# Kernel optimization log

Measured on AMD Instinct MI355X. Metric: run time of the kernel, lower is better.

## Reference

```python
import jax, jax.numpy as jnp
import numpy as np

B, IN, ED, PW, OUT, CL, NK = 2048, 4096, 8192, 2048, 256, 16, 32
MIX = 0.5

def _onehot_mask(key, n):
    # near-one-hot selector matrix [n, NK], as built by forward_update_masks
    idx = jax.random.choice(key, n, (NK,), replace=False)
    return jnp.zeros((n, NK), jnp.float32).at[idx, jnp.arange(NK)].set(1.0)

def setup_inputs():
    ks = jax.random.split(jax.random.key(0), 24)
    f = jnp.float32
    adj = (jax.random.uniform(ks[4], (IN, IN)) < 0.01).astype(f)
    adj = jnp.maximum(adj, adj.T).at[jnp.arange(IN), jnp.arange(IN)].set(1.0)
    return {
        'x_gene': jax.random.normal(ks[0], (B, IN), f),
        'x_invmea': jax.random.normal(ks[1], (B, IN), f),
        'x_curv': jax.random.normal(ks[2], (B, ED), f),
        'clinn': jax.random.normal(ks[3], (B, CL), f),
        'Adj': adj,
        'edge_mask': (jax.random.uniform(ks[5], (ED, IN)) < 0.005).astype(f),
        'pathway_mask': (jax.random.uniform(ks[6], (PW, ED)) < 0.02).astype(f),
        'top_gene_mask': _onehot_mask(ks[7], IN),
        'top_invmea_mask': _onehot_mask(ks[8], IN),
        'top_curv_mask': _onehot_mask(ks[9], ED),
        'top_path_mask': _onehot_mask(ks[10], PW),
        'W1': jnp.full((IN, IN), 0.05, f),
        'b1': 0.01 * jax.random.normal(ks[11], (IN,), f),
        'W2': jnp.full((ED, IN), 0.05, f),
        'b2': 0.01 * jax.random.normal(ks[12], (ED,), f),
        'W3': jnp.full((PW, ED), 0.05, f),
        'b3': 0.01 * jax.random.normal(ks[13], (PW,), f),
        'W4': 0.02 * jax.random.normal(ks[14], (OUT, PW), f),
        'b4': 0.01 * jax.random.normal(ks[15], (OUT,), f),
        'W5': 0.02 * jax.random.normal(ks[16], (OUT, OUT), f),
        'b5': 0.01 * jax.random.normal(ks[17], (OUT,), f),
        'W6': 0.05 * jax.random.normal(ks[18], (OUT, OUT + CL + 4 * NK), f),
        'W7': 0.05 * jax.random.normal(ks[19], (1, OUT), f),
        'mp11': MIX * jnp.ones(IN, f),
        'mp12': (1.0 - MIX) * jnp.ones(IN, f),
        'mp1': jnp.ones(IN, f),
        'mp21': MIX * jnp.ones(ED, f),
        'mp22': (1.0 - MIX) * jnp.ones(ED, f),
        'mp2': jnp.ones(ED, f),
        'mp3': jnp.ones(PW, f),
    }

def reference(x_gene, x_invmea, x_curv, clinn, Adj, edge_mask, pathway_mask,
              top_gene_mask, top_invmea_mask, top_curv_mask, top_path_mask,
              W1, b1, W2, b2, W3, b3, W4, b4, W5, b5, W6, W7,
              mp11, mp12, mp1, mp21, mp22, mp2, mp3):
    sg = jax.lax.stop_gradient
    sig = jax.nn.sigmoid
    kept_gene = sg(x_gene @ top_gene_mask)                     # [B,NK] gather-as-matmul
    x1 = sig(x_gene @ (W1 * Adj).T + b1)                       # masked linear [B,IN]
    x1 = x_invmea * (mp11 * mp1) + x1 * (mp12 * mp1)
    kept_invmea = sg(x1 @ top_invmea_mask)
    x1 = sig(x1 @ (W2 * edge_mask).T + b2)                     # [B,ED]
    x1 = x_curv * (mp21 * mp2) + x1 * (mp22 * mp2)
    kept_curv = sg(x1 @ top_curv_mask)
    x1 = sig(x1 @ (W3 * pathway_mask).T + b3)                  # [B,PW]
    x1 = x1 * mp3
    kept_path = sg(x1 @ top_path_mask)
    x1 = sig(x1 @ W4.T + b4)
    x1 = sig(x1 @ W5.T + b5)                                   # [B,OUT]
    x_cat = jnp.concatenate([x1, kept_gene, kept_invmea, kept_curv, kept_path, clinn], axis=1)
    lp = sig(x_cat @ W6.T)
    lp = lp - jnp.mean(lp, axis=1, keepdims=True)
    return lp @ W7.T                                           # [B,1]
```

## Files before the change

### kernel.cpp

```cpp
#include <hip/hip_runtime.h>

typedef unsigned short u16;
typedef __attribute__((ext_vector_type(4))) float f32x4;
typedef __attribute__((ext_vector_type(8))) short s16x8;

__device__ __forceinline__ u16 f2bf(float f) {
    union { float f; unsigned u; } c; c.f = f;
    return (u16)((c.u + 0x7fffu + ((c.u >> 16) & 1u)) >> 16);
}
__device__ __forceinline__ float bf2f(u16 u) {
    union { unsigned u; float f; } c; c.u = ((unsigned)u) << 16; return c.f;
}
__device__ __forceinline__ unsigned pk2(float a, float b) {
    return (unsigned)f2bf(a) | ((unsigned)f2bf(b) << 16);
}
__device__ __forceinline__ float sigm(float x) { return 1.0f / (1.0f + __expf(-x)); }
__device__ __forceinline__ void fma2(unsigned xv, float w, float& a0, float& a1) {
    union { float f; unsigned u; } lo, hi;
    lo.u = xv << 16; hi.u = xv & 0xFFFF0000u;
    a0 += w * lo.f; a1 += w * hi.f;
}

__device__ __forceinline__ void load16_g2l(const void* g, void* l) {
    __builtin_amdgcn_global_load_lds(
        (const __attribute__((address_space(1))) unsigned int*)(unsigned long long)g,
        (__attribute__((address_space(3))) unsigned int*)(unsigned int)(unsigned long long)l,
        16, 0, 0);
}

__device__ void d_transpF(const float* __restrict__ in, u16* __restrict__ out,
                          int Rr, int Cc, int bx, int by, float (*t)[65]) {
    const int r0 = by * 64, c0 = bx * 64;
    const int tid = threadIdx.x;
#pragma unroll
    for (int i = 0; i < 16; i++) {
        int idx = tid + i * 256;
        int rr = idx >> 6, cc = idx & 63;
        t[rr][cc] = in[(size_t)(r0 + rr) * Cc + c0 + cc];
    }
    __syncthreads();
#pragma unroll
    for (int i = 0; i < 16; i++) {
        int idx = tid + i * 256;
        int cc = idx >> 6, rr = idx & 63;
        out[(size_t)(c0 + cc) * Rr + r0 + rr] = f2bf(t[rr][cc]);
    }
}

__device__ void d_find(const float* __restrict__ mask, int n, int* __restrict__ outp,
                       int* red, int k) {
    int best = -1;
    for (int i = threadIdx.x; i < n; i += 256)
        if (mask[(size_t)i * 32 + k] != 0.0f) best = i;
    red[threadIdx.x] = best;
    __syncthreads();
    for (int off = 128; off > 0; off >>= 1) {
        if (threadIdx.x < off) {
            int o = red[threadIdx.x + off];
            if (o > red[threadIdx.x]) red[threadIdx.x] = o;
        }
        __syncthreads();
    }
    if (threadIdx.x == 0) *outp = red[0] < 0 ? 0 : red[0];
}

__device__ void d_conv(const float* __restrict__ in, u16* __restrict__ out,
                       int bid, unsigned n8) {
    unsigned i = bid * 256u + threadIdx.x;
    if (i >= n8) return;
    float4 a = ((const float4*)in)[2 * i];
    float4 b = ((const float4*)in)[2 * i + 1];
    uint4 o;
    o.x = pk2(a.x, a.y); o.y = pk2(a.z, a.w);
    o.z = pk2(b.x, b.y); o.w = pk2(b.z, b.w);
    ((uint4*)out)[i] = o;
}

template <int SUBC>
__device__ void d_ell_row(const float* __restrict__ M, const float* __restrict__ W,
                          unsigned* __restrict__ ell, int* __restrict__ cnt,
                          int PAD, int row, int* __restrict__ lds) {
    const int lane = threadIdx.x & 63;
    const int wv = threadIdx.x >> 6;
    const int C = SUBC * 4096;
    const float4* mrow = (const float4*)(M + (size_t)row * C);
    const float4* wrow = (const float4*)(W + (size_t)row * C);
    unsigned* erow = ell + (size_t)row * PAD;

    float4 m[SUBC * 4];
#pragma unroll
    for (int k = 0; k < SUBC * 4; k++) {
        int sc = k >> 2, i = k & 3;
        m[k] = mrow[(wv * SUBC + sc) * 256 + lane + i * 64];
    }
    unsigned bits[SUBC];
    int total = 0;
#pragma unroll
    for (int sc = 0; sc < SUBC; sc++) {
        unsigned b = 0;
#pragma unroll
        for (int i = 0; i < 4; i++) {
            const float4 mm = m[sc * 4 + i];
            if (mm.x != 0.f) b |= 1u << (4 * i);
            if (mm.y != 0.f) b |= 2u << (4 * i);
            if (mm.z != 0.f) b |= 4u << (4 * i);
            if (mm.w != 0.f) b |= 8u << (4 * i);
        }
        bits[sc] = b;
        total += __popc(b);
    }
    float4 w[SUBC * 4];
#pragma unroll
    for (int k = 0; k < SUBC * 4; k++) {
        int sc = k >> 2, i = k & 3;
        if ((bits[sc] >> (4 * i)) & 0xFu)
            w[k] = wrow[(wv * SUBC + sc) * 256 + lane + i * 64];
    }
    int pre = total;
#pragma unroll
    for (int off = 1; off < 64; off <<= 1) {
        int t = __shfl_up(pre, off, 64);
        if (lane >= off) pre += t;
    }
    if (lane == 63) lds[wv] = pre;
    __syncthreads();
    int base = 0;
#pragma unroll
    for (int v = 0; v < 3; v++) if (v < wv) base += lds[v];
    int s = base + pre - total;
    __asm__ volatile("" ::: "memory");
#pragma unroll
    for (int sc = 0; sc < SUBC; sc++) {
        const unsigned b = bits[sc];
        const int f4b = (wv * SUBC + sc) * 256;
#pragma unroll
        for (int i = 0; i < 4; i++) {
            if ((b >> (4 * i)) & 0xFu) {
                const float4 wv4 = w[sc * 4 + i];
                int c = (f4b + lane + i * 64) * 4;
                if (b & (1u << (4 * i))) { if (s < PAD) erow[s] = ((unsigned)f2bf(wv4.x) << 16) | (unsigned)(c + 0); s++; }
                if (b & (2u << (4 * i))) { if (s < PAD) erow[s] = ((unsigned)f2bf(wv4.y) << 16) | (unsigned)(c + 1); s++; }
                if (b & (4u << (4 * i))) { if (s < PAD) erow[s] = ((unsigned)f2bf(wv4.z) << 16) | (unsigned)(c + 2); s++; }
                if (b & (8u << (4 * i))) { if (s < PAD) erow[s] = ((unsigned)f2bf(wv4.w) << 16) | (unsigned)(c + 3); s++; }
            }
        }
    }
    if (threadIdx.x == 0) {
        int rt = lds[0] + lds[1] + lds[2] + lds[3];
        cnt[row] = rt > PAD ? PAD : rt;
    }
}

__global__ __launch_bounds__(256) void prep_all(
    const float* __restrict__ Adj, const float* __restrict__ W1,
    unsigned* __restrict__ ell1, int* __restrict__ cnt1,
    const float* __restrict__ edge, const float* __restrict__ W2,
    unsigned* __restrict__ ell2, int* __restrict__ cnt2,
    const float* __restrict__ path, const float* __restrict__ W3,
    unsigned* __restrict__ ell3, int* __restrict__ cnt3,
    const float* __restrict__ xg_f, const float* __restrict__ xinv_f,
    const float* __restrict__ xcv_f,
    u16* __restrict__ xTg, u16* __restrict__ xinvT, u16* __restrict__ xcvT,
    const float* __restrict__ m0, const float* __restrict__ m1,
    const float* __restrict__ m2, const float* __restrict__ m3,
    int* __restrict__ idx,
    const float* __restrict__ W4, u16* __restrict__ w4b,
    const float* __restrict__ W5, u16* __restrict__ w5b) {
    __shared__ float tile[64][65];
    const long long T = 22944, E = 14336;
    const int b = blockIdx.x;
    const int ea = (int)(((long long)b * E) / T);
    const int eb = (int)(((long long)(b + 1) * E) / T);
    if (eb > ea) {
        int id = ea;
        if (id < 4096) { d_ell_row<1>(Adj, W1, ell1, cnt1, 256, id, (int*)tile); return; }
        id -= 4096;
        if (id < 8192) { d_ell_row<1>(edge, W2, ell2, cnt2, 96, id, (int*)tile); return; }
        d_ell_row<2>(path, W3, ell3, cnt3, 320, id - 8192, (int*)tile);
        return;
    }
    int id = b - ea;
    if (id < 2048) { d_transpF(xg_f, xTg, 2048, 4096, id & 63, id >> 6, tile); return; }
    id -= 2048;
    if (id < 2048) { d_transpF(xinv_f, xinvT, 2048, 4096, id & 63, id >> 6, tile); return; }
    id -= 2048;
    if (id < 4096) { d_transpF(xcv_f, xcvT, 2048, 8192, id & 127, id >> 7, tile); return; }
    id -= 4096;
    if (id < 128) {
        const float* mk; int n;
        int which = id >> 5;
        if (which == 0)      { mk = m0; n = 4096; }
        else if (which == 1) { mk = m1; n = 4096; }
        else if (which == 2) { mk = m2; n = 8192; }
        else                 { mk = m3; n = 2048; }
        d_find(mk, n, idx + which * 32 + (id & 31), (int*)tile, id & 31);
        return;
    }
    id -= 128;
    if (id < 256) { d_conv(W4, w4b, id, 65536u); return; }
    id -= 256;
    d_conv(W5, w5b, id, 8192u);
}

template <int BPL>
__global__ __launch_bounds__(256) void spmm(const unsigned* __restrict__ ell,
                                            const int* __restrict__ cnt,
                                            const u16* __restrict__ xT,
                                            u16* __restrict__ outT,
                                            const float* __restrict__ bias,
                                            const float* __restrict__ c1a,
                                            const float* __restrict__ c1b,
                                            const float* __restrict__ c2a,
                                            const float* __restrict__ c2b,
                                            const u16* __restrict__ invT,
                                            const int* __restrict__ gidx,
                                            u16* __restrict__ gdst,
                                            int PAD) {
    const int lane = threadIdx.x & 63;
    const int wv = __builtin_amdgcn_readfirstlane((int)(threadIdx.x >> 6));
    const int j = blockIdx.y * 4 + wv;
    const int b0 = blockIdx.x * (64 * BPL) + lane * BPL;

    const unsigned* ep = ell + (size_t)j * PAD;
    int len = cnt[j];
    if (len > PAD) len = PAD;

    float acc[BPL];
#pragma unroll
    for (int i = 0; i < BPL; i++) acc[i] = 0.f;

    const int nfull = len >> 3;
    unsigned eA[8];
    if (nfull > 0) {
#pragma unroll
        for (int t = 0; t < 8; t++) eA[t] = ep[t];
    }
    for (int g = 0; g < nfull; g++) {
        unsigned eB[8];
        const bool more = (g + 1 < nfull);
        if (more) {
#pragma unroll
            for (int t = 0; t < 8; t++) eB[t] = ep[(g + 1) * 8 + t];
        }
        if (BPL == 8) {
            uint4 xv[8];
#pragma unroll
            for (int t = 0; t < 8; t++)
                xv[t] = *(const uint4*)(xT + ((size_t)(eA[t] & 0xFFFFu) << 11) + b0);
#pragma unroll
            for (int t = 0; t < 8; t++) {
                union { float f; unsigned u; } w; w.u = (eA[t] >> 16) << 16;
                fma2(xv[t].x, w.f, acc[0], acc[1]);
                fma2(xv[t].y, w.f, acc[2], acc[3]);
                fma2(xv[t].z, w.f, acc[4], acc[5]);
                fma2(xv[t].w, w.f, acc[6], acc[7]);
            }
        } else {
            uint2 xv[8];
#pragma unroll
            for (int t = 0; t < 8; t++)
                xv[t] = *(const uint2*)(xT + ((size_t)(eA[t] & 0xFFFFu) << 11) + b0);
#pragma unroll
            for (int t = 0; t < 8; t++) {
                union { float f; unsigned u; } w; w.u = (eA[t] >> 16) << 16;
                fma2(xv[t].x, w.f, acc[0], acc[1]);
                fma2(xv[t].y, w.f, acc[2], acc[3]);
            }
        }
        if (more) {
#pragma unroll
            for (int t = 0; t < 8; t++) eA[t] = eB[t];
        }
    }
    for (int s = nfull * 8; s < len; ++s) {
        unsigned e = ep[s];
        union { float f; unsigned u; } w; w.u = (e >> 16) << 16;
        const u16* xp = xT + ((size_t)(e & 0xFFFFu) << 11) + b0;
        if (BPL == 8) {
            uint4 xv = *(const uint4*)xp;
            fma2(xv.x, w.f, acc[0], acc[1]); fma2(xv.y, w.f, acc[2], acc[3]);
            fma2(xv.z, w.f, acc[4], acc[5]); fma2(xv.w, w.f, acc[6], acc[7]);
        } else {
            uint2 xv = *(const uint2*)xp;
            fma2(xv.x, w.f, acc[0], acc[1]); fma2(xv.y, w.f, acc[2], acc[3]);
        }
    }

    const float bi = bias[j];
    float c1 = 0.f;
    if (c1a) { c1 = c1a[j]; if (c1b) c1 *= c1b[j]; }
    float c2 = 1.f;
    if (c2a) { c2 = c2a[j]; if (c2b) c2 *= c2b[j]; }

    float v[BPL];
#pragma unroll
    for (int i = 0; i < BPL; i++) v[i] = sigm(acc[i] + bi) * c2;
    if (invT) {
        const unsigned long long* ip = (const unsigned long long*)(invT + ((size_t)j << 11) + b0);
#pragma unroll
        for (int h = 0; h < BPL / 4; h++) {
            unsigned long long iv = __builtin_nontemporal_load(ip + h);
            unsigned lo = (unsigned)iv, hi = (unsigned)(iv >> 32);
            union { float f; unsigned u; } g0, g1, g2, g3;
            g0.u = lo << 16; g1.u = lo & 0xFFFF0000u;
            g2.u = hi << 16; g3.u = hi & 0xFFFF0000u;
            v[4 * h + 0] += g0.f * c1; v[4 * h + 1] += g1.f * c1;
            v[4 * h + 2] += g2.f * c1; v[4 * h + 3] += g3.f * c1;
        }
    }
    unsigned long long pkv[BPL / 4];
#pragma unroll
    for (int h = 0; h < BPL / 4; h++)
        pkv[h] = (unsigned long long)pk2(v[4 * h + 0], v[4 * h + 1])
               | ((unsigned long long)pk2(v[4 * h + 2], v[4 * h + 3]) << 32);
    unsigned long long* op = (unsigned long long*)(outT + ((size_t)j << 11) + b0);
#pragma unroll
    for (int h = 0; h < BPL / 4; h++) __builtin_nontemporal_store(pkv[h], op + h);

    if (gdst) {
        for (int t = 0; t < 32; t++) {
            if (gidx[t] == j) {
                unsigned long long* gp = (unsigned long long*)(gdst + t * 2048 + b0);
#pragma unroll
                for (int h = 0; h < BPL / 4; h++) gp[h] = pkv[h];
            }
        }
    }
}

__global__ __launch_bounds__(256) void gatherFT(const float* __restrict__ src, int ld,
                                                const int* __restrict__ idx,
                                                u16* __restrict__ dstT) {
    int i = blockIdx.x * 256 + threadIdx.x;
    int kk = i >> 11, b = i & 2047;
    dstT[i] = f2bf(src[(size_t)b * ld + idx[kk]]);
}

__global__ __launch_bounds__(256) void transpB(const u16* __restrict__ in,
                                               u16* __restrict__ out, int Rr, int Cc) {
    __shared__ u16 t[64][66];
    const int r0 = blockIdx.y * 64, c0 = blockIdx.x * 64;
    const int tid = threadIdx.x;
#pragma unroll
    for (int i = 0; i < 16; i++) {
        int idx = tid + i * 256;
        int rr = idx >> 6, cc = idx & 63;
        t[rr][cc] = in[(size_t)(r0 + rr) * Cc + c0 + cc];
    }
    __syncthreads();
#pragma unroll
    for (int i = 0; i < 16; i++) {
        int idx = tid + i * 256;
        int cc = idx >> 6, rr = idx & 63;
        out[(size_t)(c0 + cc) * Rr + r0 + rr] = t[rr][cc];
    }
}

template <int WR, int WC, int MF, int NF, int KC, int WPE>
__global__ __launch_bounds__(WR * WC * 64, WPE)
void gemm_t(const u16* __restrict__ A, const u16* __restrict__ W,
            u16* __restrict__ Out, const float* __restrict__ bias, int N, int K) {
    constexpr int NTHR = WR * WC * 64;
    constexpr int BM = WR * MF * 16;
    constexpr int BN = WC * NF * 16;
    constexpr int BK = KC * 32;
    constexpr int CPR = KC * 4;
    constexpr int MSK = CPR - 1;
    constexpr int CA = BM * CPR / NTHR;
    constexpr int CB = BN * CPR / NTHR;
    constexpr int L  = CA + CB;

    __shared__ u16 At[2][BM * BK];
    __shared__ u16 Bt[2][BN * BK];

    const int tid = threadIdx.x;
    const int lane = tid & 63;
    const int wave = tid >> 6;
    const int wr = wave / WC, wc = wave % WC;
    const int tn = blockIdx.x, tm = blockIdx.y;
    const int r16 = lane & 15;
    const int q = lane >> 4;

    const u16* aSrc[CA]; int aDst[CA];
#pragma unroll
    for (int j = 0; j < CA; j++) {
        int c = tid + j * NTHR;
        int r = c / CPR, p = c - r * CPR;
        aSrc[j] = A + (size_t)(tm * BM + r) * K + (p ^ (r & MSK)) * 8;
        aDst[j] = c * 8;
    }
    const u16* bSrc[CB]; int bDst[CB];
#pragma unroll
    for (int j = 0; j < CB; j++) {
        int c = tid + j * NTHR;
        int r = c / CPR, p = c - r * CPR;
        bSrc[j] = W + (size_t)(tn * BN + r) * K + (p ^ (r & MSK)) * 8;
        bDst[j] = c * 8;
    }
    int aRd[MF][KC], bRd[NF][KC];
#pragma unroll
    for (int mi = 0; mi < MF; mi++)
#pragma unroll
        for (int kc = 0; kc < KC; kc++)
            aRd[mi][kc] = (wr * MF * 16 + mi * 16 + r16) * BK + (((kc * 4 + q) ^ (r16 & MSK)) << 3);
#pragma unroll
    for (int ni = 0; ni < NF; ni++)
#pragma unroll
        for (int kc = 0; kc < KC; kc++)
            bRd[ni][kc] = (wc * NF * 16 + ni * 16 + r16) * BK + (((kc * 4 + q) ^ (r16 & MSK)) << 3);

    const int nIter = K / BK;

#define ISSUE(slot, it_)                                              \
    do {                                                              \
        const int k0_ = (it_) * BK;                                   \
        _Pragma("unroll")                                             \
        for (int j = 0; j < CA; j++)                                  \
            load16_g2l(aSrc[j] + k0_, &At[slot][aDst[j]]);            \
        _Pragma("unroll")                                             \
        for (int j = 0; j < CB; j++)                                  \
            load16_g2l(bSrc[j] + k0_, &Bt[slot][bDst[j]]);            \
    } while (0)

    ISSUE(0, 0);
    if (nIter > 1) ISSUE(1, 1);

    f32x4 acc[MF][NF];
#pragma unroll
    for (int i = 0; i < MF; i++)
#pragma unroll
        for (int j = 0; j < NF; j++) acc[i][j] = (f32x4){0.f, 0.f, 0.f, 0.f};

    for (int it = 0; it < nIter; ++it) {
        const int s = it & 1;
        if (it + 1 < nIter) __builtin_amdgcn_s_waitcnt(0xF70 | L);
        else                __builtin_amdgcn_s_waitcnt(0xF70);
        __asm__ volatile("" ::: "memory");
        __builtin_amdgcn_s_barrier();
        __asm__ volatile("" ::: "memory");

        s16x8 af[KC][MF], bfr[KC][NF];
#pragma unroll
        for (int kc = 0; kc < KC; kc++) {
#pragma unroll
            for (int mi = 0; mi < MF; mi++) af[kc][mi] = *(const s16x8*)(&At[s][aRd[mi][kc]]);
#pragma unroll
            for (int ni = 0; ni < NF; ni++) bfr[kc][ni] = *(const s16x8*)(&Bt[s][bRd[ni][kc]]);
        }
        __asm__ volatile("" ::: "memory");
        __builtin_amdgcn_s_waitcnt(0xC07F);
        __builtin_amdgcn_s_barrier();
        __asm__ volatile("" ::: "memory");

        if (it + 2 < nIter) ISSUE(s, it + 2);

#pragma unroll
        for (int kc = 0; kc < KC; kc++)
#pragma unroll
            for (int mi = 0; mi < MF; mi++)
#pragma unroll
                for (int ni = 0; ni < NF; ni++)
                    acc[mi][ni] = __builtin_amdgcn_mfma_f32_16x16x32_bf16(af[kc][mi], bfr[kc][ni], acc[mi][ni], 0, 0, 0);
    }
#undef ISSUE

#pragma unroll
    for (int ni = 0; ni < NF; ni++) {
        const int n = tn * BN + wc * NF * 16 + ni * 16 + r16;
        const float bi = bias ? bias[n] : 0.f;
#pragma unroll
        for (int mi = 0; mi < MF; mi++) {
#pragma unroll
            for (int rg = 0; rg < 4; rg++) {
                const int m = tm * BM + wr * MF * 16 + mi * 16 + q * 4 + rg;
                Out[(size_t)m * N + n] = f2bf(sigm(acc[mi][ni][rg] + bi));
            }
        }
    }
}

__global__ __launch_bounds__(256) void tail_k(const u16* __restrict__ x5,
                                              const u16* __restrict__ kgT,
                                              const u16* __restrict__ kiT,
                                              const u16* __restrict__ kcT,
                                              const u16* __restrict__ kpT,
                                              const float* __restrict__ clinn,
                                              const float* __restrict__ W6,
                                              const float* __restrict__ W7,
                                              float* __restrict__ out) {
    __shared__ float xs[8 * 400];
    __shared__ float s1[4][8], s2[4][8], s3[4];
    const int tid = threadIdx.x;
    const int b0 = blockIdx.x * 8;
    for (int i = tid; i < 8 * 400; i += 256) {
        int r = i / 400, c = i - r * 400;
        int b = b0 + r;
        float v;
        if (c < 256)      v = bf2f(x5[b * 256 + c]);
        else if (c < 288) v = bf2f(kgT[(c - 256) * 2048 + b]);
        else if (c < 320) v = bf2f(kiT[(c - 288) * 2048 + b]);
        else if (c < 352) v = bf2f(kcT[(c - 320) * 2048 + b]);
        else if (c < 384) v = bf2f(kpT[(c - 352) * 2048 + b]);
        else              v = clinn[b * 16 + (c - 384)];
        xs[i] = v;
    }
    __syncthreads();
    const int j = tid;
    float acc[8];
#pragma unroll
    for (int r = 0; r < 8; r++) acc[r] = 0.f;
    const float4* wrow = (const float4*)(W6 + (size_t)j * 400);
    for (int c = 0; c < 100; c++) {
        float4 wv = wrow[c];
        const float* wp = (const float*)&wv;
#pragma unroll
        for (int t = 0; t < 4; t++) {
            float w = wp[t];
            int k = c * 4 + t;
#pragma unroll
            for (int r = 0; r < 8; r++) acc[r] += w * xs[r * 400 + k];
        }
    }
    const float w7j = W7[j];
    const int lane = tid & 63, wave = tid >> 6;
    float t3 = w7j;
#pragma unroll
    for (int off = 32; off > 0; off >>= 1) t3 += __shfl_down(t3, off, 64);
    if (lane == 0) s3[wave] = t3;
#pragma unroll
    for (int r = 0; r < 8; r++) {
        float lp = sigm(acc[r]);
        float t1 = lp, t2 = lp * w7j;
#pragma unroll
        for (int off = 32; off > 0; off >>= 1) {
            t1 += __shfl_down(t1, off, 64);
            t2 += __shfl_down(t2, off, 64);
        }
        if (lane == 0) { s1[wave][r] = t1; s2[wave][r] = t2; }
    }
    __syncthreads();
    if (tid < 8) {
        float S1 = s1[0][tid] + s1[1][tid] + s1[2][tid] + s1[3][tid];
        float S2 = s2[0][tid] + s2[1][tid] + s2[2][tid] + s2[3][tid];
        float SW = s3[0] + s3[1] + s3[2] + s3[3];
        out[b0 + tid] = S2 - (S1 * (1.f / 256.f)) * SW;
    }
}

extern "C" void kernel_launch(void* const* d_in, const int* in_sizes, int n_in,
                              void* d_out, int out_size, void* d_ws, size_t ws_size,
                              hipStream_t stream) {
    const float* x_gene   = (const float*)d_in[0];
    const float* x_invmea = (const float*)d_in[1];
    const float* x_curv   = (const float*)d_in[2];
    const float* clinn    = (const float*)d_in[3];
    const float* Adj      = (const float*)d_in[4];
    const float* edge_m   = (const float*)d_in[5];
    const float* path_m   = (const float*)d_in[6];
    const float* tg_mask  = (const float*)d_in[7];
    const float* ti_mask  = (const float*)d_in[8];
    const float* tc_mask  = (const float*)d_in[9];
    const float* tp_mask  = (const float*)d_in[10];
    const float* W1 = (const float*)d_in[11];  const float* b1 = (const float*)d_in[12];
    const float* W2 = (const float*)d_in[13];  const float* b2 = (const float*)d_in[14];
    const float* W3 = (const float*)d_in[15];  const float* b3 = (const float*)d_in[16];
    const float* W4 = (const float*)d_in[17];  const float* b4 = (const float*)d_in[18];
    const float* W5 = (const float*)d_in[19];  const float* b5 = (const float*)d_in[20];
    const float* W6 = (const float*)d_in[21];
    const float* W7 = (const float*)d_in[22];
    const float* mp11 = (const float*)d_in[23];
    const float* mp12 = (const float*)d_in[24];
    const float* mp1  = (const float*)d_in[25];
    const float* mp21 = (const float*)d_in[26];
    const float* mp22 = (const float*)d_in[27];
    const float* mp2  = (const float*)d_in[28];
    const float* mp3  = (const float*)d_in[29];

    char* ws = (char*)d_ws;
    const float* nulf = nullptr;
    float* out = (float*)d_out;

    u16*  xTg   = (u16*)(ws + 0);
    u16*  xinvT = (u16*)(ws + 16777216);
    u16*  xcvT  = (u16*)(ws + 33554432);
    u16*  x1T   = (u16*)(ws + 67108864);
    u16*  x2T   = (u16*)(ws + 83886080);
    u16*  x3T   = (u16*)(ws + 117440512);
    u16*  x3    = (u16*)(ws + 125829120);
    unsigned* ell1 = (unsigned*)(ws + 134217728);
    unsigned* ell2 = (unsigned*)(ws + 138412032);
    unsigned* ell3 = (unsigned*)(ws + 141557760);
    int* cnt1 = (int*)(ws + 144179200);
    int* cnt2 = (int*)(ws + 144195584);
    int* cnt3 = (int*)(ws + 144228352);
    int* idxg = (int*)(ws + 144236544);
    int* idxi = idxg + 32;
    int* idxc = idxg + 64;
    int* idxp = idxg + 96;
    u16* kgT  = (u16*)(ws + 144237056);
    u16* kiT  = (u16*)(ws + 144368128);
    u16* kcT  = (u16*)(ws + 144499200);
    u16* kpT  = (u16*)(ws + 144630272);
    u16* w4b  = (u16*)(ws + 144761344);
    u16* w5b  = (u16*)(ws + 145809920);
    u16* x4   = (u16*)(ws + 145940992);
    u16* x5   = (u16*)(ws + 146989568);

    prep_all<<<22944, 256, 0, stream>>>(
        Adj, W1, ell1, cnt1, edge_m, W2, ell2, cnt2, path_m, W3, ell3, cnt3,
        x_gene, x_invmea, x_curv, xTg, xinvT, xcvT,
        tg_mask, ti_mask, tc_mask, tp_mask, idxg, W4, w4b, W5, w5b);
    gatherFT<<<256, 256, 0, stream>>>(x_gene, 4096, idxg, kgT);

    spmm<4><<<dim3(8, 1024), 256, 0, stream>>>(ell1, cnt1, xTg, x1T, b1,
                                               mp11, mp1, mp12, mp1, xinvT,
                                               idxi, kiT, 256);
    spmm<4><<<dim3(8, 2048), 256, 0, stream>>>(ell2, cnt2, x1T, x2T, b2,
                                               mp21, mp2, mp22, mp2, xcvT,
                                               idxc, kcT, 96);
    spmm<4><<<dim3(8, 512), 256, 0, stream>>>(ell3, cnt3, x2T, x3T, b3,
                                              nulf, nulf, mp3, nulf, (const u16*)nullptr,
                                              idxp, kpT, 320);
    transpB<<<dim3(32, 32), 256, 0, stream>>>(x3T, x3, 2048, 2048);

    gemm_t<2, 2, 2, 2, 2, 4><<<dim3(4, 32), 256, 0, stream>>>(x3, w4b, x4, b4, 256, 2048);
    gemm_t<2, 2, 2, 2, 2, 4><<<dim3(4, 32), 256, 0, stream>>>(x4, w5b, x5, b5, 256, 256);

    tail_k<<<256, 256, 0, stream>>>(x5, kgT, kiT, kcT, kpT, clinn, W6, W7, out);
}
```

Before: 870.8 us.

## Vectorize float transpose and add dedicated layer-3 sparse kernel with finer batch split

The float-to-bf16 transpose in prep now reads float4 and writes packed bf16 pairs, which cuts the number of memory instructions. The third sparse layer moves to a new spmm_ph kernel. In it each wave handles one output row over a 128-sample batch slice, with two samples per lane and 16-entry ELL prefetch groups. The grid is reordered so rows are the fast dimension, which changes parallelism and L2 locality for the layer with the longest rows. The generic spmm also drops its BPL==8 path and gains an unused LAYER template parameter.

Result: no change. 858.4 us (-1.4%).

```diff
diff --git a/kernel.cpp b/kernel.cpp
--- a/kernel.cpp
+++ b/kernel.cpp
@@ -33,17 +33,20 @@
     const int r0 = by * 64, c0 = bx * 64;
     const int tid = threadIdx.x;
 #pragma unroll
-    for (int i = 0; i < 16; i++) {
+    for (int i = 0; i < 4; i++) {
         int idx = tid + i * 256;
-        int rr = idx >> 6, cc = idx & 63;
-        t[rr][cc] = in[(size_t)(r0 + rr) * Cc + c0 + cc];
+        int rr = idx >> 4, c4 = (idx & 15) * 4;
+        float4 v = *(const float4*)(in + (size_t)(r0 + rr) * Cc + c0 + c4);
+        t[rr][c4 + 0] = v.x; t[rr][c4 + 1] = v.y;
+        t[rr][c4 + 2] = v.z; t[rr][c4 + 3] = v.w;
     }
     __syncthreads();
 #pragma unroll
-    for (int i = 0; i < 16; i++) {
+    for (int i = 0; i < 8; i++) {
         int idx = tid + i * 256;
-        int cc = idx >> 6, rr = idx & 63;
-        out[(size_t)(c0 + cc) * Rr + r0 + rr] = f2bf(t[rr][cc]);
+        int cc = idx >> 5, rp = (idx & 31) * 2;
+        unsigned p = pk2(t[rp][cc], t[rp + 1][cc]);
+        *(unsigned*)(out + (size_t)(c0 + cc) * Rr + r0 + rp) = p;
     }
 }
 
@@ -202,7 +205,7 @@
     d_conv(W5, w5b, id, 8192u);
 }
 
-template <int BPL>
+template <int BPL, int LAYER>
 __global__ __launch_bounds__(256) void spmm(const unsigned* __restrict__ ell,
                                             const int* __restrict__ cnt,
                                             const u16* __restrict__ xT,
@@ -242,30 +245,15 @@
 #pragma unroll
             for (int t = 0; t < 8; t++) eB[t] = ep[(g + 1) * 8 + t];
         }
-        if (BPL == 8) {
-            uint4 xv[8];
-#pragma unroll
-            for (int t = 0; t < 8; t++)
-                xv[t] = *(const uint4*)(xT + ((size_t)(eA[t] & 0xFFFFu) << 11) + b0);
-#pragma unroll
-            for (int t = 0; t < 8; t++) {
-                union { float f; unsigned u; } w; w.u = (eA[t] >> 16) << 16;
-                fma2(xv[t].x, w.f, acc[0], acc[1]);
-                fma2(xv[t].y, w.f, acc[2], acc[3]);
-                fma2(xv[t].z, w.f, acc[4], acc[5]);
-                fma2(xv[t].w, w.f, acc[6], acc[7]);
-            }
-        } else {
-            uint2 xv[8];
-#pragma unroll
-            for (int t = 0; t < 8; t++)
-                xv[t] = *(const uint2*)(xT + ((size_t)(eA[t] & 0xFFFFu) << 11) + b0);
-#pragma unroll
-            for (int t = 0; t < 8; t++) {
-                union { float f; unsigned u; } w; w.u = (eA[t] >> 16) << 16;
-                fma2(xv[t].x, w.f, acc[0], acc[1]);
-                fma2(xv[t].y, w.f, acc[2], acc[3]);
-            }
+        uint2 xv[8];
+#pragma unroll
+        for (int t = 0; t < 8; t++)
+            xv[t] = *(const uint2*)(xT + ((size_t)(eA[t] & 0xFFFFu) << 11) + b0);
+#pragma unroll
+        for (int t = 0; t < 8; t++) {
+            union { float f; unsigned u; } w; w.u = (eA[t] >> 16) << 16;
+            fma2(xv[t].x, w.f, acc[0], acc[1]);
+            fma2(xv[t].y, w.f, acc[2], acc[3]);
         }
         if (more) {
 #pragma unroll
@@ -276,14 +264,8 @@
         unsigned e = ep[s];
         union { float f; unsigned u; } w; w.u = (e >> 16) << 16;
         const u16* xp = xT + ((size_t)(e & 0xFFFFu) << 11) + b0;
-        if (BPL == 8) {
-            uint4 xv = *(const uint4*)xp;
-            fma2(xv.x, w.f, acc[0], acc[1]); fma2(xv.y, w.f, acc[2], acc[3]);
-            fma2(xv.z, w.f, acc[4], acc[5]); fma2(xv.w, w.f, acc[6], acc[7]);
-        } else {
-            uint2 xv = *(const uint2*)xp;
-            fma2(xv.x, w.f, acc[0], acc[1]); fma2(xv.y, w.f, acc[2], acc[3]);
-        }
+        uint2 xv = *(const uint2*)xp;
+        fma2(xv.x, w.f, acc[0], acc[1]); fma2(xv.y, w.f, acc[2], acc[3]);
     }
 
     const float bi = bias[j];
@@ -324,6 +306,72 @@
 #pragma unroll
                 for (int h = 0; h < BPL / 4; h++) gp[h] = pkv[h];
             }
+        }
+    }
+}
+
+__global__ __launch_bounds__(256) void spmm_ph(const unsigned* __restrict__ ell,
+                                               const int* __restrict__ cnt,
+                                               const u16* __restrict__ xT,
+                                               u16* __restrict__ outT,
+                                               const float* __restrict__ bias,
+                                               const float* __restrict__ scale,
+                                               const int* __restrict__ gidx,
+                                               u16* __restrict__ gdst,
+                                               int PAD) {
+    const int lane = threadIdx.x & 63;
+    const int wv = __builtin_amdgcn_readfirstlane((int)(threadIdx.x >> 6));
+    const int j = blockIdx.x * 4 + wv;
+    const int b0 = blockIdx.y * 128 + lane * 2;
+
+    const unsigned* ep = ell + (size_t)j * PAD;
+    int len = cnt[j];
+    if (len > PAD) len = PAD;
+
+    float a0 = 0.f, a1 = 0.f;
+    const int nfull = len >> 4;
+    unsigned eA[16];
+    if (nfull > 0) {
+#pragma unroll
+        for (int t = 0; t < 16; t++) eA[t] = ep[t];
+    }
+    for (int g = 0; g < nfull; g++) {
+        unsigned eB[16];
+        const bool more = (g + 1 < nfull);
+        if (more) {
+#pragma unroll
+            for (int t = 0; t < 16; t++) eB[t] = ep[(g + 1) * 16 + t];
+        }
+        unsigned xv[16];
+#pragma unroll
+        for (int t = 0; t < 16; t++)
+            xv[t] = *(const unsigned*)(xT + ((size_t)(eA[t] & 0xFFFFu) << 11) + b0);
+#pragma unroll
+        for (int t = 0; t < 16; t++) {
+            union { float f; unsigned u; } w; w.u = (eA[t] >> 16) << 16;
+            fma2(xv[t], w.f, a0, a1);
+        }
+        if (more) {
+#pragma unroll
+            for (int t = 0; t < 16; t++) eA[t] = eB[t];
+        }
+    }
+    for (int s = nfull * 16; s < len; ++s) {
+        unsigned e = ep[s];
+        union { float f; unsigned u; } w; w.u = (e >> 16) << 16;
+        unsigned xv = *(const unsigned*)(xT + ((size_t)(e & 0xFFFFu) << 11) + b0);
+        fma2(xv, w.f, a0, a1);
+    }
+
+    const float bi = bias[j];
+    const float sc = scale[j];
+    const unsigned pk = pk2(sigm(a0 + bi) * sc, sigm(a1 + bi) * sc);
+    *(unsigned*)(outT + ((size_t)j << 11) + b0) = pk;
+
+    if (gdst) {
+        for (int t = 0; t < 32; t++) {
+            if (gidx[t] == j)
+                *(unsigned*)(gdst + t * 2048 + b0) = pk;
         }
     }
 }
@@ -612,15 +660,14 @@
         tg_mask, ti_mask, tc_mask, tp_mask, idxg, W4, w4b, W5, w5b);
     gatherFT<<<256, 256, 0, stream>>>(x_gene, 4096, idxg, kgT);
 
-    spmm<4><<<dim3(8, 1024), 256, 0, stream>>>(ell1, cnt1, xTg, x1T, b1,
-                                               mp11, mp1, mp12, mp1, xinvT,
-                                               idxi, kiT, 256);
-    spmm<4><<<dim3(8, 2048), 256, 0, stream>>>(ell2, cnt2, x1T, x2T, b2,
-                                               mp21, mp2, mp22, mp2, xcvT,
-                                               idxc, kcT, 96);
-    spmm<4><<<dim3(8, 512), 256, 0, stream>>>(ell3, cnt3, x2T, x3T, b3,
-                                              nulf, nulf, mp3, nulf, (const u16*)nullptr,
-                                              idxp, kpT, 320);
+    spmm<4, 1><<<dim3(8, 1024), 256, 0, stream>>>(ell1, cnt1, xTg, x1T, b1,
+                                                  mp11, mp1, mp12, mp1, xinvT,
+                                                  idxi, kiT, 256);
+    spmm<4, 2><<<dim3(8, 2048), 256, 0, stream>>>(ell2, cnt2, x1T, x2T, b2,
+                                                  mp21, mp2, mp22, mp2, xcvT,
+                                                  idxc, kcT, 96);
+    spmm_ph<<<dim3(512, 16), 256, 0, stream>>>(ell3, cnt3, x2T, x3T, b3,
+                                               mp3, idxp, kpT, 320);
     transpB<<<dim3(32, 32), 256, 0, stream>>>(x3T, x3, 2048, 2048);
 
     gemm_t<2, 2, 2, 2, 2, 4><<<dim3(4, 32), 256, 0, stream>>>(x3, w4b, x4, b4, 256, 2048);
```
